# Kernel optimization log

Measured on AMD Instinct MI355X. Metric: run time of the kernel, lower is better.

## Reference

```python
import jax, jax.numpy as jnp
import numpy as np

THRESHOLD = 33.33  # torch forward default

def setup_inputs() -> dict:
    key = jax.random.key(0)
    k1, k2 = jax.random.split(key)
    source_pc = jax.random.normal(k1, (2, 16384, 3), dtype=jnp.float32)
    target_pc = jax.random.normal(k2, (2, 16384, 3), dtype=jnp.float32)
    return {"source_pc": source_pc, "target_pc": target_pc}

def _pairwise_dist(x, y):
    # Euclidean cdist via the matmul expansion (same math as torch.cdist p=2).
    # x: [B, N, D], y: [B, M, D] -> [B, N, M]
    x2 = jnp.sum(x * x, axis=-1)              # [B, N]
    y2 = jnp.sum(y * y, axis=-1)              # [B, M]
    xy = jnp.einsum('bnd,bmd->bnm', x, y)     # [B, N, M]
    d2 = x2[:, :, None] + y2[None if False else slice(None), None, :] - 2.0 * xy
    d2 = x2[:, :, None] + y2[:, None, :] - 2.0 * xy
    return jnp.sqrt(jnp.maximum(d2, 0.0))

def reference(source_pc, target_pc):
    dist = _pairwise_dist(source_pc.astype(jnp.float32), target_pc.astype(jnp.float32))
    dist1 = jnp.minimum(jnp.min(dist, axis=2), THRESHOLD)  # [B, N] clamped
    dist2 = jnp.minimum(jnp.min(dist, axis=1), THRESHOLD)  # [B, M] clamped
    d1 = jnp.mean(dist1, axis=-1)
    d2 = jnp.mean(dist2, axis=-1)
    return (d1 + d2) / 2.0  # bidirectional=True default -> [B]
```

## Files before the change

### kernel.cpp

```cpp
#include <hip/hip_runtime.h>

#define NPTS 16384
#define TH 33.33f

typedef __attribute__((ext_vector_type(8)))  __bf16 bf16x8;
typedef __attribute__((ext_vector_type(16))) float  f32x16;

__device__ __forceinline__ unsigned short f2bf(float x) {
    unsigned u = __float_as_uint(x);
    u += 0x7FFFu + ((u >> 16) & 1u);
    return (unsigned short)(u >> 16);
}
__device__ __forceinline__ float bf2f(unsigned short h) {
    return __uint_as_float(((unsigned)h) << 16);
}

union UV { uint4 v; bf16x8 h; unsigned short s[8]; };


#define FOLD2(MM, AA) { \
    f32x16 t0 = __builtin_amdgcn_mfma_f32_32x32x16_bf16(AA, q0, zc, 0, 0, 0); \
    f32x16 t1 = __builtin_amdgcn_mfma_f32_32x32x16_bf16(AA, q1, zc, 0, 0, 0); \
    _Pragma("unroll") for (int j = 0; j < 16; j++) MM[j] = fmaxf(fmaxf(t0[j], t1[j]), MM[j]); }

__device__ __forceinline__ void conv_store(unsigned short* lb, int k,
                                           float x, float y, float z) {
    float hp = 0.5f * fmaf(z, z, fmaf(y, y, x * x));
    unsigned short xh = f2bf(x), yh = f2bf(y), zh = f2bf(z);
    unsigned short xl = f2bf(x - bf2f(xh)), yl = f2bf(y - bf2f(yh)), zl = f2bf(z - bf2f(zh));
    float rr = hp;
    unsigned short h0 = f2bf(rr); rr -= bf2f(h0);
    unsigned short h1 = f2bf(rr); rr -= bf2f(h1);
    unsigned short h2 = f2bf(rr);
    UV c0, c1;
    c0.s[0]=xh; c0.s[1]=yh; c0.s[2]=zh; c0.s[3]=xh; c0.s[4]=yh; c0.s[5]=zh; c0.s[6]=xl; c0.s[7]=yl;
    c1.s[0]=zl; c1.s[1]=(unsigned short)(h0^0x8000); c1.s[2]=(unsigned short)(h1^0x8000);
    c1.s[3]=(unsigned short)(h2^0x8000); c1.s[4]=0; c1.s[5]=0; c1.s[6]=0; c1.s[7]=0;
    int t = k >> 5, pos = k & 31;
    *(uint4*)(lb + t * 512 + pos * 8)       = c0.v;
    *(uint4*)(lb + t * 512 + 256 + pos * 8) = c1.v;
}

#define LOAD_PTS(CC) { \
    const float* g0 = pp + (size_t)(seg * 2048 + (CC) * 512 + tid) * 3; \
    px0 = g0[0]; py0 = g0[1]; pz0 = g0[2]; \
    const float* g1 = g0 + 768; \
    px1 = g1[0]; py1 = g1[1]; pz1 = g1[2]; }

#define CONV_WRITE(BUF) { \
    unsigned short* lb = (unsigned short*)(smem + (BUF) * 16384); \
    conv_store(lb, tid,       px0, py0, pz0); \
    conv_store(lb, tid + 256, px1, py1, pz1); }

#define EPILOG(MM, P) { \
    float* sc = scratch + wave * 1056; \
    _Pragma("unroll") for (int j = 0; j < 16; j++) { \
        int r0 = (j & 3) + 8 * (j >> 2) + 4 * g; sc[r0 * 33 + cc] = MM[j]; } \
    __syncthreads(); \
    const float* sr = sc + cc * 33 + g * 16; \
    float mx = -3.0e38f; \
    _Pragma("unroll") for (int k = 0; k < 16; k++) mx = fmaxf(mx, sr[k]); \
    mx = fmaxf(mx, __shfl_xor(mx, 32, 64)); \
    if (lane < 32) { \
        float d2 = 2.0f * (hq[P] - mx); \
        float d = fminf(sqrtf(fmaxf(d2, 0.0f)), TH); \
        dst[wave * 64 + (P) * 32 + lane] = d; } \
    __syncthreads(); }

__global__ __launch_bounds__(256, 4) void chamfer_kernel(
        const float* __restrict__ src, const float* __restrict__ tgt,
        float* __restrict__ d2part, float* __restrict__ out)
{
    const int db = blockIdx.y, dir = db >> 1, b = db & 1;
    const int rowblock = blockIdx.x >> 3, seg = blockIdx.x & 7;
    const int tid = threadIdx.x, wave = tid >> 6, lane = tid & 63;
    const int g = lane >> 5, cc = lane & 31;
    if (blockIdx.x == 0 && db == 0 && tid < 2) out[tid] = 0.0f;
    const float* qp = (dir == 0 ? src : tgt) + (size_t)b * NPTS * 3;
    const float* pp = (dir == 0 ? tgt : src) + (size_t)b * NPTS * 3;
    const unsigned short one = 0x3F80;

    __shared__ alignas(16) unsigned char smem[32768];
    float* scratch = (float*)smem;

    const int rt0 = rowblock * 8 + wave * 2;
    bf16x8 afrag[2]; float hq[2];
#pragma unroll
    for (int i = 0; i < 2; i++) {
        int r = (rt0 + i) * 32 + cc;
        float x = qp[r * 3 + 0], y = qp[r * 3 + 1], z = qp[r * 3 + 2];
        hq[i] = 0.5f * fmaf(z, z, fmaf(y, y, x * x));
        unsigned short xh = f2bf(x), yh = f2bf(y), zh = f2bf(z);
        unsigned short xl = f2bf(x - bf2f(xh)), yl = f2bf(y - bf2f(yh)), zl = f2bf(z - bf2f(zh));
        UV f0, f1, rv;
        f0.s[0]=xh; f0.s[1]=yh; f0.s[2]=zh; f0.s[3]=xl; f0.s[4]=yl; f0.s[5]=zl; f0.s[6]=xh; f0.s[7]=yh;
        f1.s[0]=zh; f1.s[1]=one; f1.s[2]=one; f1.s[3]=one; f1.s[4]=0; f1.s[5]=0; f1.s[6]=0; f1.s[7]=0;
        rv.v = g ? f1.v : f0.v;
        afrag[i] = rv.h;
    }

    f32x16 m0 = -3.0e38f, m1 = -3.0e38f;
    const f32x16 zc = 0.0f;
    float px0, py0, pz0, px1, py1, pz1;

    LOAD_PTS(0)
    CONV_WRITE(0)
    __syncthreads();
#pragma unroll 1
    for (int c = 0; c < 4; ++c) {
        if (c < 3) LOAD_PTS(c + 1)
        const unsigned short* bb = (const unsigned short*)(smem + (c & 1) * 16384);
#pragma unroll 1
        for (int pt = 0; pt < 8; ++pt) {
            bf16x8 q0 = *(const bf16x8*)(bb + pt * 1024 + lane * 8);
            bf16x8 q1 = *(const bf16x8*)(bb + pt * 1024 + 512 + lane * 8);
            FOLD2(m0, afrag[0])
            FOLD2(m1, afrag[1])
        }
        if (c < 3) CONV_WRITE((c + 1) & 1)
        __syncthreads();
    }

    float* dst = d2part + (((size_t)(db * 64 + rowblock)) * 8 + seg) * 256;
    EPILOG(m0, 0)
    EPILOG(m1, 1)
}

__global__ __launch_bounds__(256) void merge_kernel(const float* __restrict__ d2part,
                                                    float* __restrict__ out) {
    const int b = blockIdx.y;
    const int slice = blockIdx.x;
    const int tid = threadIdx.x;
    float s = 0.0f;
#pragma unroll
    for (int pass = 0; pass < 2; pass++) {
        const float* base = d2part + (size_t)(pass * 2 + b) * 64 * 8 * 256;
#pragma unroll
        for (int i = 0; i < 4; i++) {
            int r = slice * 1024 + i * 256 + tid;
            const float* p = base + (size_t)(r >> 8) * 2048 + (r & 255);
            float m = p[0];
#pragma unroll
            for (int sgi = 1; sgi < 8; sgi++) m = fminf(m, p[sgi * 256]);
            s += m;
        }
    }
#pragma unroll
    for (int off = 32; off > 0; off >>= 1) s += __shfl_down(s, off, 64);
    __shared__ float w[4];
    if ((tid & 63) == 0) w[tid >> 6] = s;
    __syncthreads();
    if (tid == 0) {
        float t = (w[0] + w[1]) + (w[2] + w[3]);
        atomicAdd(&out[b], t * (1.0f / (2.0f * NPTS)));
    }
}

extern "C" void kernel_launch(void* const* d_in, const int* in_sizes, int n_in,
                              void* d_out, int out_size, void* d_ws, size_t ws_size,
                              hipStream_t stream) {
    const float* src = (const float*)d_in[0];
    const float* tgt = (const float*)d_in[1];
    float* out = (float*)d_out;
    float* d2part = (float*)d_ws;

    chamfer_kernel<<<dim3(512, 4), 256, 0, stream>>>(src, tgt, d2part, out);
    merge_kernel<<<dim3(16, 2), 256, 0, stream>>>(d2part, out);
}
```

Measured before the change: 91.62 us.

## Compute both Chamfer directions from one distance pass with column partial maxima

Adds a symmetric kernel that computes each source-target distance tile once. It reduces the tile over rows to get per-target partial minima, written to a large workspace, while still reducing over columns for source minima. This halves the MFMA work compared with running each direction separately. In exchange it adds an extra cross-lane reduction and a global store per tile, plus a merge kernel that must read about 32 MB of column partials. The new path runs only when the workspace is large enough; otherwise the old two-direction path is used.

```diff
diff --git a/kernel.cpp b/kernel.cpp
--- a/kernel.cpp
+++ b/kernel.cpp
@@ -18,10 +18,11 @@
 union UV { uint4 v; bf16x8 h; unsigned short s[8]; };
 
 
-#define FOLD2(MM, AA) { \
-    f32x16 t0 = __builtin_amdgcn_mfma_f32_32x32x16_bf16(AA, q0, zc, 0, 0, 0); \
-    f32x16 t1 = __builtin_amdgcn_mfma_f32_32x32x16_bf16(AA, q1, zc, 0, 0, 0); \
-    _Pragma("unroll") for (int j = 0; j < 16; j++) MM[j] = fmaxf(fmaxf(t0[j], t1[j]), MM[j]); }
+#define LOAD_PTS(CC) { \
+    const float* g0 = pp + (size_t)(seg * 2048 + (CC) * 512 + tid) * 3; \
+    px0 = g0[0]; py0 = g0[1]; pz0 = g0[2]; \
+    const float* g1 = g0 + 768; \
+    px1 = g1[0]; py1 = g1[1]; pz1 = g1[2]; }
 
 __device__ __forceinline__ void conv_store(unsigned short* lb, int k,
                                            float x, float y, float z) {
@@ -41,11 +42,10 @@
     *(uint4*)(lb + t * 512 + 256 + pos * 8) = c1.v;
 }
 
-#define LOAD_PTS(CC) { \
-    const float* g0 = pp + (size_t)(seg * 2048 + (CC) * 512 + tid) * 3; \
-    px0 = g0[0]; py0 = g0[1]; pz0 = g0[2]; \
-    const float* g1 = g0 + 768; \
-    px1 = g1[0]; py1 = g1[1]; pz1 = g1[2]; }
+#define FOLD2(MM, AA) { \
+    f32x16 t0 = __builtin_amdgcn_mfma_f32_32x32x16_bf16(AA, q0, zc, 0, 0, 0); \
+    f32x16 t1 = __builtin_amdgcn_mfma_f32_32x32x16_bf16(AA, q1, zc, 0, 0, 0); \
+    _Pragma("unroll") for (int j = 0; j < 16; j++) MM[j] = fmaxf(fmaxf(t0[j], t1[j]), MM[j]); }
 
 #define CONV_WRITE(BUF) { \
     unsigned short* lb = (unsigned short*)(smem + (BUF) * 16384); \
@@ -156,14 +156,201 @@
     }
 }
 
+__device__ __forceinline__ void conv_store_sym(unsigned short* lb, int k,
+                                               float x, float y, float z) {
+    float hp = 0.5f * fmaf(z, z, fmaf(y, y, x * x));
+    unsigned short xh = f2bf(x), yh = f2bf(y), zh = f2bf(z);
+    unsigned short xl = f2bf(x - bf2f(xh)), yl = f2bf(y - bf2f(yh)), zl = f2bf(z - bf2f(zh));
+    float rr = hp;
+    unsigned short h0 = f2bf(rr); rr -= bf2f(h0);
+    unsigned short h1 = f2bf(rr); rr -= bf2f(h1);
+    unsigned short h2 = f2bf(rr);
+    const unsigned short one = 0x3F80;
+    UV c0, c1;
+    c0.s[0]=xh; c0.s[1]=yh; c0.s[2]=zh; c0.s[3]=xh; c0.s[4]=yh; c0.s[5]=zh; c0.s[6]=xl; c0.s[7]=yl;
+    c1.s[0]=zl; c1.s[1]=(unsigned short)(h0^0x8000); c1.s[2]=(unsigned short)(h1^0x8000);
+    c1.s[3]=(unsigned short)(h2^0x8000); c1.s[4]=one; c1.s[5]=one; c1.s[6]=one; c1.s[7]=0;
+    int t = k >> 5, pos = k & 31;
+    *(uint4*)(lb + t * 512 + pos * 8)       = c0.v;
+    *(uint4*)(lb + t * 512 + 256 + pos * 8) = c1.v;
+}
+
+#define CONV_WRITE_SYM(BUF) { \
+    unsigned short* lb = (unsigned short*)(smem + (BUF) * 16384); \
+    conv_store_sym(lb, tid,       px0, py0, pz0); \
+    conv_store_sym(lb, tid + 256, px1, py1, pz1); }
+
+#define EPILOG_SYM(MM, P) { \
+    float* sc = scratch + wave * 1056; \
+    _Pragma("unroll") for (int j = 0; j < 16; j++) { \
+        int r0 = (j & 3) + 8 * (j >> 2) + 4 * g; sc[r0 * 33 + cc] = MM[j]; } \
+    __syncthreads(); \
+    const float* sr = sc + cc * 33 + g * 16; \
+    float mx = -3.0e38f; \
+    _Pragma("unroll") for (int k = 0; k < 16; k++) mx = fmaxf(mx, sr[k]); \
+    mx = fmaxf(mx, __shfl_xor(mx, 32, 64)); \
+    if (lane < 32) { \
+        float d2 = -2.0f * mx; \
+        float d = fminf(sqrtf(fmaxf(d2, 0.0f)), TH); \
+        dst[wave * 64 + (P) * 32 + lane] = d; } \
+    __syncthreads(); }
+
+__global__ __launch_bounds__(256, 4) void chamfer_sym(
+        const float* __restrict__ src, const float* __restrict__ tgt,
+        float* __restrict__ rowpart, float* __restrict__ colpart,
+        float* __restrict__ out)
+{
+    const int b = blockIdx.y;
+    const int rowblock = blockIdx.x >> 3, seg = blockIdx.x & 7;
+    const int tid = threadIdx.x, wave = tid >> 6, lane = tid & 63;
+    const int g = lane >> 5, cc = lane & 31;
+    if (blockIdx.x == 0 && b == 0 && tid < 2) out[tid] = 0.0f;
+    const float* qp = src + (size_t)b * NPTS * 3;
+    const float* pp = tgt + (size_t)b * NPTS * 3;
+    const unsigned short one = 0x3F80;
+
+    __shared__ alignas(16) unsigned char smem[32768];
+    float* scratch = (float*)smem;
+
+    const int rt0 = rowblock * 8 + wave * 2;
+    bf16x8 afrag[2];
+#pragma unroll
+    for (int i = 0; i < 2; i++) {
+        int r = (rt0 + i) * 32 + cc;
+        float x = qp[r * 3 + 0], y = qp[r * 3 + 1], z = qp[r * 3 + 2];
+        float hqv = 0.5f * fmaf(z, z, fmaf(y, y, x * x));
+        unsigned short xh = f2bf(x), yh = f2bf(y), zh = f2bf(z);
+        unsigned short xl = f2bf(x - bf2f(xh)), yl = f2bf(y - bf2f(yh)), zl = f2bf(z - bf2f(zh));
+        float rr = hqv;
+        unsigned short q0h = f2bf(rr); rr -= bf2f(q0h);
+        unsigned short q1h = f2bf(rr); rr -= bf2f(q1h);
+        unsigned short q2h = f2bf(rr);
+        UV f0, f1, rv;
+        f0.s[0]=xh; f0.s[1]=yh; f0.s[2]=zh; f0.s[3]=xl; f0.s[4]=yl; f0.s[5]=zl; f0.s[6]=xh; f0.s[7]=yh;
+        f1.s[0]=zh; f1.s[1]=one; f1.s[2]=one; f1.s[3]=one;
+        f1.s[4]=(unsigned short)(q0h^0x8000); f1.s[5]=(unsigned short)(q1h^0x8000);
+        f1.s[6]=(unsigned short)(q2h^0x8000); f1.s[7]=0;
+        rv.v = g ? f1.v : f0.v;
+        afrag[i] = rv.h;
+    }
+
+    f32x16 m0 = -3.0e38f, m1 = -3.0e38f;
+    const f32x16 zc = 0.0f;
+    float px0, py0, pz0, px1, py1, pz1;
+
+    float* colw = colpart + ((size_t)(b * 64 + rowblock) * 4 + wave) * 16384 + seg * 2048;
+
+    LOAD_PTS(0)
+    CONV_WRITE_SYM(0)
+    __syncthreads();
+#pragma unroll 1
+    for (int c = 0; c < 4; ++c) {
+        if (c < 3) LOAD_PTS(c + 1)
+        const unsigned short* bb = (const unsigned short*)(smem + (c & 1) * 16384);
+        float* cw = colw + c * 512;
+#pragma unroll 1
+        for (int pt = 0; pt < 8; ++pt) {
+            bf16x8 q0 = *(const bf16x8*)(bb + pt * 1024 + lane * 8);
+            bf16x8 q1 = *(const bf16x8*)(bb + pt * 1024 + 512 + lane * 8);
+            float cv0, cv1;
+            {
+                f32x16 t0 = __builtin_amdgcn_mfma_f32_32x32x16_bf16(afrag[0], q0, zc, 0, 0, 0);
+                f32x16 t1 = __builtin_amdgcn_mfma_f32_32x32x16_bf16(afrag[0], q1, zc, 0, 0, 0);
+#pragma unroll
+                for (int j = 0; j < 16; j++) m0[j] = fmaxf(fmaxf(t0[j], t1[j]), m0[j]);
+                cv0 = fmaxf(t0[0], t0[1]); cv1 = fmaxf(t1[0], t1[1]);
+#pragma unroll
+                for (int j = 2; j < 16; j += 2) {
+                    cv0 = fmaxf(fmaxf(t0[j], t0[j + 1]), cv0);
+                    cv1 = fmaxf(fmaxf(t1[j], t1[j + 1]), cv1);
+                }
+            }
+            {
+                f32x16 t0 = __builtin_amdgcn_mfma_f32_32x32x16_bf16(afrag[1], q0, zc, 0, 0, 0);
+                f32x16 t1 = __builtin_amdgcn_mfma_f32_32x32x16_bf16(afrag[1], q1, zc, 0, 0, 0);
+#pragma unroll
+                for (int j = 0; j < 16; j++) m1[j] = fmaxf(fmaxf(t0[j], t1[j]), m1[j]);
+#pragma unroll
+                for (int j = 0; j < 16; j += 2) {
+                    cv0 = fmaxf(fmaxf(t0[j], t0[j + 1]), cv0);
+                    cv1 = fmaxf(fmaxf(t1[j], t1[j + 1]), cv1);
+                }
+            }
+            cv0 = fmaxf(cv0, __shfl_xor(cv0, 32, 64));
+            cv1 = fmaxf(cv1, __shfl_xor(cv1, 32, 64));
+            cw[pt * 64 + lane] = g ? cv1 : cv0;
+        }
+        if (c < 3) CONV_WRITE_SYM((c + 1) & 1)
+        __syncthreads();
+    }
+
+    float* dst = rowpart + (((size_t)(b * 64 + rowblock)) * 8 + seg) * 256;
+    EPILOG_SYM(m0, 0)
+    EPILOG_SYM(m1, 1)
+}
+
+__global__ __launch_bounds__(256) void merge_sym(const float* __restrict__ rowpart,
+                                                 const float* __restrict__ colpart,
+                                                 float* __restrict__ out)
+{
+    const int b = blockIdx.y;
+    const int x = blockIdx.x;
+    const int tid = threadIdx.x;
+    __shared__ float sh[128];
+    __shared__ float w[4];
+    float s = 0.0f;
+    if (x < 128) {
+        const int col = x * 128 + (tid & 127);
+        const int half = tid >> 7;
+        const float* p = colpart + ((size_t)b * 256 + (size_t)half * 128) * 16384 + col;
+        float m = -3.0e38f;
+#pragma unroll 8
+        for (int i = 0; i < 128; i++) m = fmaxf(m, p[(size_t)i * 16384]);
+        if (half) sh[tid & 127] = m;
+        __syncthreads();
+        if (!half) {
+            m = fmaxf(m, sh[tid]);
+            s = fminf(sqrtf(fmaxf(-2.0f * m, 0.0f)), TH);
+        }
+    } else {
+        const int rb4 = x - 128;
+        const float* base = rowpart + (size_t)b * 64 * 8 * 256;
+#pragma unroll
+        for (int i = 0; i < 16; i++) {
+            int r = rb4 * 4096 + i * 256 + tid;
+            const float* p = base + (size_t)(r >> 8) * 2048 + (r & 255);
+            float m = p[0];
+#pragma unroll
+            for (int sgi = 1; sgi < 8; sgi++) m = fminf(m, p[sgi * 256]);
+            s += m;
+        }
+    }
+#pragma unroll
+    for (int off = 32; off > 0; off >>= 1) s += __shfl_down(s, off, 64);
+    if ((tid & 63) == 0) w[tid >> 6] = s;
+    __syncthreads();
+    if (tid == 0)
+        atomicAdd(&out[b], (w[0] + w[1] + w[2] + w[3]) * (1.0f / (2.0f * NPTS)));
+}
+
 extern "C" void kernel_launch(void* const* d_in, const int* in_sizes, int n_in,
                               void* d_out, int out_size, void* d_ws, size_t ws_size,
                               hipStream_t stream) {
     const float* src = (const float*)d_in[0];
     const float* tgt = (const float*)d_in[1];
     float* out = (float*)d_out;
-    float* d2part = (float*)d_ws;
-
-    chamfer_kernel<<<dim3(512, 4), 256, 0, stream>>>(src, tgt, d2part, out);
-    merge_kernel<<<dim3(16, 2), 256, 0, stream>>>(d2part, out);
-}
+
+    const size_t COLPART_BYTES = (size_t)2 * 64 * 4 * 16384 * 4;
+    const size_t ROWPART_BYTES = (size_t)2 * 64 * 8 * 256 * 4;
+
+    if (ws_size >= COLPART_BYTES + ROWPART_BYTES) {
+        float* colpart = (float*)d_ws;
+        float* rowpart = (float*)((char*)d_ws + COLPART_BYTES);
+        chamfer_sym<<<dim3(512, 2), 256, 0, stream>>>(src, tgt, rowpart, colpart, out);
+        merge_sym<<<dim3(132, 2), 256, 0, stream>>>(rowpart, colpart, out);
+    } else {
+        float* d2part = (float*)d_ws;
+        chamfer_kernel<<<dim3(512, 4), 256, 0, stream>>>(src, tgt, d2part, out);
+        merge_kernel<<<dim3(16, 2), 256, 0, stream>>>(d2part, out);
+    }
+}
```

Result: slower. 118.1 us (+28.9%).
